# Kernel tuning notes

Hardware: AMD Instinct MI355X
Metric: run time of the kernel (lower is better)

## Reference

```python
import jax, jax.numpy as jnp
import numpy as np

LATENT, HIDDEN, OUT = 256, 1024, 512
B, T = 32, 512
NUM_LAYERS = 3


def setup_inputs() -> dict:
    key = jax.random.key(0)
    ks = jax.random.split(key, 16)
    init = lambda k, shape, fan: (jax.random.normal(k, shape, jnp.float32) / np.sqrt(fan)).astype(jnp.float32)
    seq_lens = jnp.sort(jax.random.randint(ks[2], (B,), 1, T + 1)).at[-1].set(T)
    inp = {
        "z": jax.random.normal(ks[0], (B, LATENT), jnp.float32),
        "seq_lens": seq_lens,
        "chord_embedding": jax.random.normal(ks[1], (B, T, HIDDEN), jnp.float32),
        "fc_w": init(ks[3], (HIDDEN, LATENT), LATENT),
        "fc_b": jnp.zeros((HIDDEN,), jnp.float32),
    }
    in_dims = [HIDDEN, OUT, OUT]
    for l in range(NUM_LAYERS):
        inp[f"w_ih{l}"] = init(ks[4 + 2 * l], (3 * OUT, in_dims[l]), in_dims[l])
        inp[f"w_hh{l}"] = init(ks[5 + 2 * l], (3 * OUT, OUT), OUT)
        inp[f"b_ih{l}"] = jnp.zeros((3 * OUT,), jnp.float32)
        inp[f"b_hh{l}"] = jnp.zeros((3 * OUT,), jnp.float32)
    return inp


def _gru_layer(x, w_ih, w_hh, b_ih, b_hh):
    # x: [B, T, in_dim] -> [B, T, H]; PyTorch gate order: r, z, n
    Bb, Tt, _ = x.shape
    H = w_hh.shape[1]
    gx = jnp.einsum('bti,gi->btg', x, w_ih) + b_ih  # [B, T, 3H] batched GEMM

    def step(h, gx_t):
        gh = h @ w_hh.T + b_hh                      # [B, 3H]
        xr, xz, xn = jnp.split(gx_t, 3, axis=-1)
        hr, hz, hn = jnp.split(gh, 3, axis=-1)
        r = jax.nn.sigmoid(xr + hr)
        zg = jax.nn.sigmoid(xz + hz)
        n = jnp.tanh(xn + r * hn)
        h_new = (1.0 - zg) * n + zg * h
        return h_new, h_new

    h0 = jnp.zeros((Bb, H), x.dtype)
    _, ys = jax.lax.scan(step, h0, jnp.swapaxes(gx, 0, 1))  # scan over time
    return jnp.swapaxes(ys, 0, 1)


def reference(z, seq_lens, chord_embedding, fc_w, fc_b,
              w_ih0, w_hh0, b_ih0, b_hh0,
              w_ih1, w_hh1, b_ih1, b_hh1,
              w_ih2, w_hh2, b_ih2, b_hh2):
    # FC + ReLU, broadcast over time, add scaled chord embedding
    h = jax.nn.relu(z @ fc_w.T + fc_b)[:, None, :]          # [B, 1, HIDDEN]
    x = h + chord_embedding / 100.0                          # [B, T, HIDDEN]
    # 3-layer GRU, batched over all samples at once. GRU is causal, so running
    # the full padded sequence and masking t >= seq_len equals the original
    # per-sample truncated loop (positions < seq_len are bitwise identical).
    x = _gru_layer(x, w_ih0, w_hh0, b_ih0, b_hh0)
    x = _gru_layer(x, w_ih1, w_hh1, b_ih1, b_hh1)
    x = _gru_layer(x, w_ih2, w_hh2, b_ih2, b_hh2)
    mask = (jnp.arange(x.shape[1])[None, :] < seq_lens[:, None]).astype(x.dtype)
    return x * mask[:, :, None]                              # [B, T, OUT], zero-padded
```

## Files before the change

### kernel.cpp

```cpp
#include <hip/hip_runtime.h>
#include <hip/hip_bf16.h>
#include <stdint.h>

#define LATENT 256
#define HIDDEN 1024
#define GOUT 512
#define NB 32
#define TT 512
#define G3 1536

typedef float f32x4 __attribute__((ext_vector_type(4)));
typedef short s16x8 __attribute__((ext_vector_type(8)));
typedef uint32_t u32;
typedef unsigned long long u64;

#define GLP(p) ((const __attribute__((address_space(1))) u32*)(p))
#define LLP(p) ((__attribute__((address_space(3))) u32*)(p))

__device__ __forceinline__ short f2bf(float f) {
  u32 u = __builtin_bit_cast(u32, f);
  u32 r = (u + 0x7FFFu + ((u >> 16) & 1u)) >> 16;
  return (short)r;
}
__device__ __forceinline__ float bf2f(short s) {
  u32 u = ((u32)(unsigned short)s) << 16;
  return __builtin_bit_cast(float, u);
}
__device__ __forceinline__ u32 pk2(float a, float b) {
  return (u32)(unsigned short)f2bf(a) | ((u32)(unsigned short)f2bf(b) << 16);
}
__device__ __forceinline__ s16x8 f2bf8(float4 a, float4 b) {
  s16x8 r;
  r[0] = f2bf(a.x); r[1] = f2bf(a.y); r[2] = f2bf(a.z); r[3] = f2bf(a.w);
  r[4] = f2bf(b.x); r[5] = f2bf(b.y); r[6] = f2bf(b.z); r[7] = f2bf(b.w);
  return r;
}
__device__ __forceinline__ float ldgx(const float* p) { return *p; }
__device__ __forceinline__ float ldgx(const short* p) { return bf2f(*p); }

__global__ __launch_bounds__(256) void fc_kernel(const float* __restrict__ z,
                                                 const float* __restrict__ fc_w,
                                                 const float* __restrict__ fc_b,
                                                 float* __restrict__ hfc) {
  __shared__ float zs[LATENT];
  int tid = threadIdx.x;
  int gid = blockIdx.x * 256 + tid;
  int b = gid >> 10, j = gid & 1023;
  zs[tid] = z[b * LATENT + tid];
  __syncthreads();
  const float4* wr = (const float4*)(fc_w + (size_t)j * LATENT);
  float s = 0.f;
#pragma unroll
  for (int k = 0; k < LATENT / 4; ++k) {
    float4 wv = wr[k];
    float4 zv = *(const float4*)&zs[k * 4];
    s += wv.x * zv.x + wv.y * zv.y + wv.z * zv.z + wv.w * zv.w;
  }
  s += fc_b[j];
  hfc[gid] = fmaxf(s, 0.f);
}

__global__ __launch_bounds__(256) void x0_kernel(const float* __restrict__ hfc,
                                                 const float* __restrict__ chord,
                                                 short* __restrict__ x0) {
  int r = blockIdx.x;
  int b = r & 31, t = r >> 5;
  int k = threadIdx.x * 4;
  float4 c = *(const float4*)(chord + ((size_t)b * TT + t) * HIDDEN + k);
  float4 h = *(const float4*)(hfc + (size_t)b * HIDDEN + k);
  u32 p0 = pk2(h.x + c.x * 0.01f, h.y + c.y * 0.01f);
  u32 p1 = pk2(h.z + c.z * 0.01f, h.w + c.w * 0.01f);
  uint2 pv; pv.x = p0; pv.y = p1;
  *(uint2*)(x0 + (size_t)r * HIDDEN + k) = pv;
}

__global__ __launch_bounds__(256) void cvt_kernel(const float* __restrict__ src,
                                                  short* __restrict__ dst, int n4) {
  int i = blockIdx.x * 256 + threadIdx.x;
  if (i < n4) {
    float4 v = ((const float4*)src)[i];
    uint2 pv; pv.x = pk2(v.x, v.y); pv.y = pk2(v.z, v.w);
    ((uint2*)dst)[i] = pv;
  }
}

template <typename OutT>
__global__ __launch_bounds__(256) void gemm_bt(const short* __restrict__ A,
                                               const short* __restrict__ Bw,
                                               OutT* __restrict__ C, int M, int N, int K) {
  __shared__ short As[128 * 32];
  __shared__ short Bs[128 * 32];
  const int tid = threadIdx.x;
  const int lane = tid & 63, wave = tid >> 6;
  const int l15 = lane & 15, quad = lane >> 4;
  const int n0 = blockIdx.x * 128, m0 = blockIdx.y * 128;
  const int wm = (wave >> 1) * 64, wn = (wave & 1) * 64;
  f32x4 acc[4][4] = {};
  for (int k0 = 0; k0 < K; k0 += 32) {
#pragma unroll
    for (int c = 0; c < 2; ++c) {
      int idx = c * 256 + tid;
      int row = idx >> 2, cs = (idx & 3) * 8;
      const u32* ga = (const u32*)(A + (size_t)(m0 + row) * K + k0 + cs);
      const u32* gb = (const u32*)(Bw + (size_t)(n0 + row) * K + k0 + cs);
      u32* sa = (u32*)As + (size_t)(c * 256 + wave * 64) * 4;
      u32* sb = (u32*)Bs + (size_t)(c * 256 + wave * 64) * 4;
      __builtin_amdgcn_global_load_lds(GLP(ga), LLP(sa), 16, 0, 0);
      __builtin_amdgcn_global_load_lds(GLP(gb), LLP(sb), 16, 0, 0);
    }
    __syncthreads();
    s16x8 af[4], bfr[4];
#pragma unroll
    for (int i = 0; i < 4; ++i)
      af[i] = *(const s16x8*)(As + (wm + i * 16 + l15) * 32 + quad * 8);
#pragma unroll
    for (int j = 0; j < 4; ++j)
      bfr[j] = *(const s16x8*)(Bs + (wn + j * 16 + l15) * 32 + quad * 8);
#pragma unroll
    for (int i = 0; i < 4; ++i)
#pragma unroll
      for (int j = 0; j < 4; ++j)
        acc[i][j] = __builtin_amdgcn_mfma_f32_16x16x32_bf16(af[i], bfr[j], acc[i][j], 0, 0, 0);
    __syncthreads();
  }
#pragma unroll
  for (int i = 0; i < 4; ++i)
#pragma unroll
    for (int j = 0; j < 4; ++j)
#pragma unroll
      for (int r = 0; r < 4; ++r) {
        int m = m0 + wm + i * 16 + quad * 4 + r;
        int n = n0 + wn + j * 16 + l15;
        float v = acc[i][j][r];
        if constexpr (__is_same(OutT, float)) C[(size_t)m * N + n] = v;
        else C[(size_t)m * N + n] = f2bf(v);
      }
}

template <typename GxT>
__global__ __launch_bounds__(512) void gru_layer(const GxT* __restrict__ gx,
                                                 const float* __restrict__ w_hh,
                                                 const float* __restrict__ b_ih,
                                                 const float* __restrict__ b_hh,
                                                 u64* __restrict__ h_buf,
                                                 int tag_base,
                                                 short* __restrict__ x_out,
                                                 float* __restrict__ f_out,
                                                 const int* __restrict__ seq_lens) {
  const int bid = blockIdx.x;
  const int g = bid & 7, wg = bid >> 3;
  const int u0 = wg * 32;
  const int tid = threadIdx.x, lane = tid & 63, wave = tid >> 6;
  const int l15 = lane & 15, quad = lane >> 4;
  __shared__ u32 h_lds[4 * 256];
  __shared__ float lds_c[3 * 4 * 32];

  u64* hb = h_buf + (size_t)g * 2048;

  const int gate = wave >> 1, half = wave & 1;
  s16x8 wfrag[16];
  if (wave < 6) {
    const int col = gate * 512 + u0 + half * 16 + l15;
#pragma unroll
    for (int kb = 0; kb < 16; ++kb) {
      const float* p = w_hh + (size_t)col * 512 + kb * 32 + quad * 8;
      wfrag[kb] = f2bf8(*(const float4*)p, *(const float4*)(p + 4));
    }
  }

  const bool is_c = (wave >= 6);
  const int ci = tid - 384;
  const int cb = ci >> 5, cu = ci & 31;
  const int gbat = g * 4 + cb, u = u0 + cu;
  float bihr = 0, bihz = 0, bihn = 0, bhhr = 0, bhhz = 0, bhhn = 0;
  int slen = 0;
  float hprev = 0.f, pgx[3] = {0.f, 0.f, 0.f};
  if (is_c) {
    bihr = b_ih[u]; bihz = b_ih[512 + u]; bihn = b_ih[1024 + u];
    bhhr = b_hh[u]; bhhz = b_hh[512 + u]; bhhn = b_hh[1024 + u];
    slen = seq_lens[gbat];
#pragma unroll
    for (int gs = 0; gs < 3; ++gs)
      pgx[gs] = ldgx(&gx[(size_t)gbat * G3 + gs * 512 + u]);
  }

  const int w0 = tid * 2;
  const int srow = w0 >> 8, sc = w0 & 255;
  const int saddr = srow * 256 + (sc ^ (srow * 4) ^ ((srow & 1) * 16));

  for (int t = 0; t < TT; ++t) {
    if (t > 0) {
      const u32 want = (u32)(tag_base + t);
      u64* src = hb + ((t - 1) & 1) * 1024;
      u64 v0 = __hip_atomic_load(src + w0, __ATOMIC_RELAXED, __HIP_MEMORY_SCOPE_AGENT);
      u64 v1 = __hip_atomic_load(src + w0 + 1, __ATOMIC_RELAXED, __HIP_MEMORY_SCOPE_AGENT);
      while ((u32)(v0 >> 32) != want)
        v0 = __hip_atomic_load(src + w0, __ATOMIC_RELAXED, __HIP_MEMORY_SCOPE_AGENT);
      while ((u32)(v1 >> 32) != want)
        v1 = __hip_atomic_load(src + w0 + 1, __ATOMIC_RELAXED, __HIP_MEMORY_SCOPE_AGENT);
      uint2 pw; pw.x = (u32)v0; pw.y = (u32)v1;
      *(uint2*)&h_lds[saddr] = pw;
    }
    __syncthreads();

    if (wave < 6) {
      f32x4 a0 = {0.f, 0.f, 0.f, 0.f}, a1 = a0, a2 = a0, a3 = a0;
      if (t > 0) {
        const int r = l15 & 3;
        const int rsw = r * 4, rhi = (r & 1) * 16;
#pragma unroll
        for (int kb = 0; kb < 16; ++kb) {
          s16x8 a = *(const s16x8*)&h_lds[r * 256 + ((kb * 16 + quad * 4) ^ rsw ^ rhi)];
          if ((kb & 3) == 0)      a0 = __builtin_amdgcn_mfma_f32_16x16x32_bf16(a, wfrag[kb], a0, 0, 0, 0);
          else if ((kb & 3) == 1) a1 = __builtin_amdgcn_mfma_f32_16x16x32_bf16(a, wfrag[kb], a1, 0, 0, 0);
          else if ((kb & 3) == 2) a2 = __builtin_amdgcn_mfma_f32_16x16x32_bf16(a, wfrag[kb], a2, 0, 0, 0);
          else                    a3 = __builtin_amdgcn_mfma_f32_16x16x32_bf16(a, wfrag[kb], a3, 0, 0, 0);
        }
      }
      if (quad == 0) {
        const int uc = half * 16 + l15;
#pragma unroll
        for (int r = 0; r < 4; ++r)
          lds_c[gate * 128 + r * 32 + uc] = (a0[r] + a1[r]) + (a2[r] + a3[r]);
      }
    }
    __syncthreads();

    if (is_c) {
      float ghr = lds_c[0 * 128 + cb * 32 + cu];
      float ghz = lds_c[1 * 128 + cb * 32 + cu];
      float ghn = lds_c[2 * 128 + cb * 32 + cu];
      float cr = pgx[0], cz = pgx[1], cn = pgx[2];
      if (t + 1 < TT) {
#pragma unroll
        for (int gs = 0; gs < 3; ++gs)
          pgx[gs] = ldgx(&gx[(size_t)((t + 1) * NB + gbat) * G3 + gs * 512 + u]);
      }
      float xr = cr + bihr + ghr + bhhr;
      float xz = cz + bihz + ghz + bhhz;
      float rr = 1.f / (1.f + __expf(-xr));
      float zz = 1.f / (1.f + __expf(-xz));
      float pre = cn + bihn + rr * (ghn + bhhn);
      float ax = fabsf(pre);
      float e = __expf(-2.f * ax);
      float nn = copysignf((1.f - e) / (1.f + e), pre);
      float h = (1.f - zz) * nn + zz * hprev;
      hprev = h;
      float other = __shfl_xor(h, 1);
      if (!(tid & 1)) {
        u64 val = (u64)pk2(h, other) | (((u64)(u32)(tag_base + t + 1)) << 32);
        __hip_atomic_store(hb + (t & 1) * 1024 + cb * 256 + (u >> 1), val,
                           __ATOMIC_RELAXED, __HIP_MEMORY_SCOPE_AGENT);
      }
      if (x_out) x_out[(size_t)(t * NB + gbat) * 512 + u] = f2bf(h);
      if (f_out) f_out[((size_t)gbat * TT + t) * 512 + u] = (t < slen) ? h : 0.f;
    }
  }
}

extern "C" void kernel_launch(void* const* d_in, const int* in_sizes, int n_in,
                              void* d_out, int out_size, void* d_ws, size_t ws_size,
                              hipStream_t stream) {
  (void)in_sizes; (void)n_in; (void)out_size;
  const float* z       = (const float*)d_in[0];
  const int*   seq     = (const int*)d_in[1];
  const float* chord   = (const float*)d_in[2];
  const float* fc_w    = (const float*)d_in[3];
  const float* fc_b    = (const float*)d_in[4];
  const float* w_ih[3] = {(const float*)d_in[5], (const float*)d_in[9],  (const float*)d_in[13]};
  const float* w_hh[3] = {(const float*)d_in[6], (const float*)d_in[10], (const float*)d_in[14]};
  const float* b_ih[3] = {(const float*)d_in[7], (const float*)d_in[11], (const float*)d_in[15]};
  const float* b_hh[3] = {(const float*)d_in[8], (const float*)d_in[12], (const float*)d_in[16]};

  char* w = (char*)d_ws;
  size_t off = 0;
  auto alloc = [&](size_t bytes) -> void* {
    void* p = w + off;
    off = (off + bytes + 255) & ~(size_t)255;
    return p;
  };
  u64*   hbuf = (u64*)alloc((size_t)8 * 2048 * 8);
  float* hfc  = (float*)alloc((size_t)NB * HIDDEN * 4);
  short* x0   = (short*)alloc((size_t)TT * NB * HIDDEN * 2);
  short* x1   = (short*)alloc((size_t)TT * NB * GOUT * 2);
  short* w0b  = (short*)alloc((size_t)G3 * HIDDEN * 2);
  short* w1b  = (short*)alloc((size_t)G3 * GOUT * 2);
  short* w2b  = (short*)alloc((size_t)G3 * GOUT * 2);
  size_t fixed = off;
  bool gx_f32 = (fixed + (size_t)TT * NB * G3 * 4) <= ws_size;
  void* gx = alloc(gx_f32 ? (size_t)TT * NB * G3 * 4 : (size_t)TT * NB * G3 * 2);

  fc_kernel<<<128, 256, 0, stream>>>(z, fc_w, fc_b, hfc);
  x0_kernel<<<TT * NB, 256, 0, stream>>>(hfc, chord, x0);
  cvt_kernel<<<(G3 * HIDDEN / 4 + 255) / 256, 256, 0, stream>>>(w_ih[0], w0b, G3 * HIDDEN / 4);
  cvt_kernel<<<(G3 * GOUT / 4 + 255) / 256, 256, 0, stream>>>(w_ih[1], w1b, G3 * GOUT / 4);
  cvt_kernel<<<(G3 * GOUT / 4 + 255) / 256, 256, 0, stream>>>(w_ih[2], w2b, G3 * GOUT / 4);

  dim3 gg(G3 / 128, TT * NB / 128);
  if (gx_f32) {
    float* gxf = (float*)gx;
    gemm_bt<float><<<gg, 256, 0, stream>>>(x0, w0b, gxf, TT * NB, G3, HIDDEN);
    gru_layer<float><<<128, 512, 0, stream>>>(gxf, w_hh[0], b_ih[0], b_hh[0], hbuf, 0 * 1024, x1, nullptr, seq);
    gemm_bt<float><<<gg, 256, 0, stream>>>(x1, w1b, gxf, TT * NB, G3, GOUT);
    gru_layer<float><<<128, 512, 0, stream>>>(gxf, w_hh[1], b_ih[1], b_hh[1], hbuf, 1 * 1024, x1, nullptr, seq);
    gemm_bt<float><<<gg, 256, 0, stream>>>(x1, w2b, gxf, TT * NB, G3, GOUT);
    gru_layer<float><<<128, 512, 0, stream>>>(gxf, w_hh[2], b_ih[2], b_hh[2], hbuf, 2 * 1024, nullptr, (float*)d_out, seq);
  } else {
    short* gxb = (short*)gx;
    gemm_bt<short><<<gg, 256, 0, stream>>>(x0, w0b, gxb, TT * NB, G3, HIDDEN);
    gru_layer<short><<<128, 512, 0, stream>>>(gxb, w_hh[0], b_ih[0], b_hh[0], hbuf, 0 * 1024, x1, nullptr, seq);
    gemm_bt<short><<<gg, 256, 0, stream>>>(x1, w1b, gxb, TT * NB, G3, GOUT);
    gru_layer<short><<<128, 512, 0, stream>>>(gxb, w_hh[1], b_ih[1], b_hh[1], hbuf, 1 * 1024, x1, nullptr, seq);
    gemm_bt<short><<<gg, 256, 0, stream>>>(x1, w2b, gxb, TT * NB, G3, GOUT);
    gru_layer<short><<<128, 512, 0, stream>>>(gxb, w_hh[2], b_ih[2], b_hh[2], hbuf, 2 * 1024, nullptr, (float*)d_out, seq);
  }
}
```

Measured before the change: 2.700 ms.

## Fuse three GRU layers into one wavefront-pipelined persistent kernel

Replaces the three sequential GRU layer kernels and the two intermediate input-projection GEMMs with one persistent kernel of 96 blocks, 32 per layer. Each layer consumes the previous layer's hidden state per timestep through tagged ring buffers with 4 slots, and layers 1-2 compute their input projection on the fly with MFMA in spare waves. This lets the layers run as a time-skewed pipeline instead of serially and drops the gx round trips to global memory. Blocks now cover 16 batch rows, so each step has fewer cross-block exchanges. In exchange it relies on all 96 blocks being co-resident, adds backpressure spinning, and increases LDS and register pressure.

```diff
diff --git a/kernel.cpp b/kernel.cpp
--- a/kernel.cpp
+++ b/kernel.cpp
@@ -37,6 +37,9 @@
 }
 __device__ __forceinline__ float ldgx(const float* p) { return *p; }
 __device__ __forceinline__ float ldgx(const short* p) { return bf2f(*p); }
+__device__ __forceinline__ u64 ald(const u64* p) {
+  return __hip_atomic_load(p, __ATOMIC_RELAXED, __HIP_MEMORY_SCOPE_AGENT);
+}
 
 __global__ __launch_bounds__(256) void fc_kernel(const float* __restrict__ z,
                                                  const float* __restrict__ fc_w,
@@ -137,123 +140,210 @@
       }
 }
 
+
+struct GruP {
+  const float* w_hh[3];
+  const float* w_ih[3];
+  const float* b_ih[3];
+  const float* b_hh[3];
+};
+
+#define SLOT_WORDS 4096
+#define HB_WORDS  (4 * SLOT_WORDS)
+
+__global__ __launch_bounds__(256) void clr_kernel(u64* __restrict__ p) {
+  p[(size_t)blockIdx.x * 256 + threadIdx.x] = 0ull;
+}
+
 template <typename GxT>
-__global__ __launch_bounds__(512) void gru_layer(const GxT* __restrict__ gx,
-                                                 const float* __restrict__ w_hh,
-                                                 const float* __restrict__ b_ih,
-                                                 const float* __restrict__ b_hh,
-                                                 u64* __restrict__ h_buf,
-                                                 int tag_base,
-                                                 short* __restrict__ x_out,
-                                                 float* __restrict__ f_out,
-                                                 const int* __restrict__ seq_lens) {
+__global__ __launch_bounds__(1024) void gru3(GruP P,
+                                             const GxT* __restrict__ gx0,
+                                             u64* __restrict__ hbc,
+                                             const int* __restrict__ seq,
+                                             float* __restrict__ out) {
   const int bid = blockIdx.x;
-  const int g = bid & 7, wg = bid >> 3;
+  const int layer = bid >> 5;
+  const int g = bid & 1;
+  const int wg = (bid >> 1) & 15;
   const int u0 = wg * 32;
-  const int tid = threadIdx.x, lane = tid & 63, wave = tid >> 6;
+  const int tid = threadIdx.x;
+  const int lane = tid & 63, wave = tid >> 6;
   const int l15 = lane & 15, quad = lane >> 4;
-  __shared__ u32 h_lds[4 * 256];
-  __shared__ float lds_c[3 * 4 * 32];
-
-  u64* hb = h_buf + (size_t)g * 2048;
-
-  const int gate = wave >> 1, half = wave & 1;
+
+  __shared__ u32 h_lds[16 * 256];
+  __shared__ u32 x_lds[16 * 256];
+  __shared__ float gh_c[3 * 512];
+  __shared__ float gx_c[3 * 512];
+
+  u64* hb_own = hbc + (size_t)(layer * 2 + g) * HB_WORDS;
+  const u64* hb_prev = (layer > 0) ? hbc + (size_t)((layer - 1) * 2 + g) * HB_WORDS : hbc;
+  const u64* hb_next = (layer < 2) ? hbc + (size_t)((layer + 1) * 2 + g) * HB_WORDS : hbc;
+
+  const bool is_hh = (wave < 6);
+  const bool do_ih = (wave >= 6 && wave < 12 && layer > 0);
+  const bool is_c  = (wave >= 12);
+
+  int gate = 0, half = 0;
   s16x8 wfrag[16];
-  if (wave < 6) {
+  if (is_hh || do_ih) {
+    const int wv = is_hh ? wave : wave - 6;
+    gate = wv >> 1; half = wv & 1;
+    const float* W = is_hh ? P.w_hh[layer] : P.w_ih[layer];
     const int col = gate * 512 + u0 + half * 16 + l15;
 #pragma unroll
     for (int kb = 0; kb < 16; ++kb) {
-      const float* p = w_hh + (size_t)col * 512 + kb * 32 + quad * 8;
+      const float* p = W + (size_t)col * 512 + kb * 32 + quad * 8;
       wfrag[kb] = f2bf8(*(const float4*)p, *(const float4*)(p + 4));
     }
   }
 
-  const bool is_c = (wave >= 6);
-  const int ci = tid - 384;
-  const int cb = ci >> 5, cu = ci & 31;
-  const int gbat = g * 4 + cb, u = u0 + cu;
-  float bihr = 0, bihz = 0, bihn = 0, bhhr = 0, bhhz = 0, bhhn = 0;
-  int slen = 0;
-  float hprev = 0.f, pgx[3] = {0.f, 0.f, 0.f};
+  const int ci0 = tid - 768;
+  float bih[2][3], bhh[2][3], pgx[2][3], hprev[2];
+  int slen[2];
+  hprev[0] = hprev[1] = 0.f; slen[0] = slen[1] = 0;
+#pragma unroll
+  for (int p = 0; p < 2; ++p)
+#pragma unroll
+    for (int gs = 0; gs < 3; ++gs) { bih[p][gs] = 0.f; bhh[p][gs] = 0.f; pgx[p][gs] = 0.f; }
   if (is_c) {
-    bihr = b_ih[u]; bihz = b_ih[512 + u]; bihn = b_ih[1024 + u];
-    bhhr = b_hh[u]; bhhz = b_hh[512 + u]; bhhn = b_hh[1024 + u];
-    slen = seq_lens[gbat];
-#pragma unroll
-    for (int gs = 0; gs < 3; ++gs)
-      pgx[gs] = ldgx(&gx[(size_t)gbat * G3 + gs * 512 + u]);
-  }
-
-  const int w0 = tid * 2;
-  const int srow = w0 >> 8, sc = w0 & 255;
-  const int saddr = srow * 256 + (sc ^ (srow * 4) ^ ((srow & 1) * 16));
+#pragma unroll
+    for (int p = 0; p < 2; ++p) {
+      const int ci = ci0 + p * 256;
+      const int cu = ci & 31, cb = ci >> 5;
+      const int u = u0 + cu, gb = g * 16 + cb;
+#pragma unroll
+      for (int gs = 0; gs < 3; ++gs) {
+        bih[p][gs] = P.b_ih[layer][gs * 512 + u];
+        bhh[p][gs] = P.b_hh[layer][gs * 512 + u];
+      }
+      slen[p] = seq[gb];
+      if (layer == 0) {
+#pragma unroll
+        for (int gs = 0; gs < 3; ++gs)
+          pgx[p][gs] = ldgx(&gx0[(size_t)gb * G3 + gs * 512 + u]);
+      }
+    }
+  }
+
+  const int w0 = tid * 4;
+  const int srow = w0 >> 8;
+  const int saddr = srow * 256 + ((w0 & 255) ^ (srow << 2));
 
   for (int t = 0; t < TT; ++t) {
+    const bool chk = (layer < 2 && t >= 4 && tid < 16);
+    const u64* cw = hb_next + (size_t)(t & 3) * SLOT_WORDS + tid * 16;
+    u64 cv = 0;
+    if (chk) cv = ald(cw);
+    const u64* hsrc = hb_own + (size_t)((t - 1) & 3) * SLOT_WORDS + w0;
+    u64 hv0 = 0, hv1 = 0, hv2 = 0, hv3 = 0;
+    if (t > 0) { hv0 = ald(hsrc); hv1 = ald(hsrc + 1); hv2 = ald(hsrc + 2); hv3 = ald(hsrc + 3); }
+    const u64* xsrc = hb_prev + (size_t)(t & 3) * SLOT_WORDS + w0;
+    u64 xv0 = 0, xv1 = 0, xv2 = 0, xv3 = 0;
+    if (layer > 0) { xv0 = ald(xsrc); xv1 = ald(xsrc + 1); xv2 = ald(xsrc + 2); xv3 = ald(xsrc + 3); }
+
+    if (chk) {
+      const u32 wt = (u32)(t - 3);
+      while ((int)((u32)(cv >> 32) - wt) < 0) cv = ald(cw);
+    }
     if (t > 0) {
-      const u32 want = (u32)(tag_base + t);
-      u64* src = hb + ((t - 1) & 1) * 1024;
-      u64 v0 = __hip_atomic_load(src + w0, __ATOMIC_RELAXED, __HIP_MEMORY_SCOPE_AGENT);
-      u64 v1 = __hip_atomic_load(src + w0 + 1, __ATOMIC_RELAXED, __HIP_MEMORY_SCOPE_AGENT);
-      while ((u32)(v0 >> 32) != want)
-        v0 = __hip_atomic_load(src + w0, __ATOMIC_RELAXED, __HIP_MEMORY_SCOPE_AGENT);
-      while ((u32)(v1 >> 32) != want)
-        v1 = __hip_atomic_load(src + w0 + 1, __ATOMIC_RELAXED, __HIP_MEMORY_SCOPE_AGENT);
-      uint2 pw; pw.x = (u32)v0; pw.y = (u32)v1;
-      *(uint2*)&h_lds[saddr] = pw;
+      const u32 wt = (u32)t;
+      while ((u32)(hv0 >> 32) != wt) hv0 = ald(hsrc);
+      while ((u32)(hv1 >> 32) != wt) hv1 = ald(hsrc + 1);
+      while ((u32)(hv2 >> 32) != wt) hv2 = ald(hsrc + 2);
+      while ((u32)(hv3 >> 32) != wt) hv3 = ald(hsrc + 3);
+      uint4 pw; pw.x = (u32)hv0; pw.y = (u32)hv1; pw.z = (u32)hv2; pw.w = (u32)hv3;
+      *(uint4*)&h_lds[saddr] = pw;
+    }
+    if (layer > 0) {
+      const u32 wt = (u32)(t + 1);
+      while ((u32)(xv0 >> 32) != wt) xv0 = ald(xsrc);
+      while ((u32)(xv1 >> 32) != wt) xv1 = ald(xsrc + 1);
+      while ((u32)(xv2 >> 32) != wt) xv2 = ald(xsrc + 2);
+      while ((u32)(xv3 >> 32) != wt) xv3 = ald(xsrc + 3);
+      uint4 pw; pw.x = (u32)xv0; pw.y = (u32)xv1; pw.z = (u32)xv2; pw.w = (u32)xv3;
+      *(uint4*)&x_lds[saddr] = pw;
     }
     __syncthreads();
 
-    if (wave < 6) {
+    if (is_hh) {
       f32x4 a0 = {0.f, 0.f, 0.f, 0.f}, a1 = a0, a2 = a0, a3 = a0;
       if (t > 0) {
-        const int r = l15 & 3;
-        const int rsw = r * 4, rhi = (r & 1) * 16;
+        const int rb = l15 * 256, rx = l15 << 2;
 #pragma unroll
         for (int kb = 0; kb < 16; ++kb) {
-          s16x8 a = *(const s16x8*)&h_lds[r * 256 + ((kb * 16 + quad * 4) ^ rsw ^ rhi)];
+          s16x8 a = *(const s16x8*)&h_lds[rb + ((kb * 16 + quad * 4) ^ rx)];
           if ((kb & 3) == 0)      a0 = __builtin_amdgcn_mfma_f32_16x16x32_bf16(a, wfrag[kb], a0, 0, 0, 0);
           else if ((kb & 3) == 1) a1 = __builtin_amdgcn_mfma_f32_16x16x32_bf16(a, wfrag[kb], a1, 0, 0, 0);
           else if ((kb & 3) == 2) a2 = __builtin_amdgcn_mfma_f32_16x16x32_bf16(a, wfrag[kb], a2, 0, 0, 0);
           else                    a3 = __builtin_amdgcn_mfma_f32_16x16x32_bf16(a, wfrag[kb], a3, 0, 0, 0);
         }
       }
-      if (quad == 0) {
-        const int uc = half * 16 + l15;
-#pragma unroll
-        for (int r = 0; r < 4; ++r)
-          lds_c[gate * 128 + r * 32 + uc] = (a0[r] + a1[r]) + (a2[r] + a3[r]);
-      }
+      const int uc = half * 16 + l15;
+#pragma unroll
+      for (int r = 0; r < 4; ++r)
+        gh_c[gate * 512 + (quad * 4 + r) * 32 + uc] = (a0[r] + a1[r]) + (a2[r] + a3[r]);
+    } else if (do_ih) {
+      f32x4 a0 = {0.f, 0.f, 0.f, 0.f}, a1 = a0, a2 = a0, a3 = a0;
+      const int rb = l15 * 256, rx = l15 << 2;
+#pragma unroll
+      for (int kb = 0; kb < 16; ++kb) {
+        s16x8 a = *(const s16x8*)&x_lds[rb + ((kb * 16 + quad * 4) ^ rx)];
+        if ((kb & 3) == 0)      a0 = __builtin_amdgcn_mfma_f32_16x16x32_bf16(a, wfrag[kb], a0, 0, 0, 0);
+        else if ((kb & 3) == 1) a1 = __builtin_amdgcn_mfma_f32_16x16x32_bf16(a, wfrag[kb], a1, 0, 0, 0);
+        else if ((kb & 3) == 2) a2 = __builtin_amdgcn_mfma_f32_16x16x32_bf16(a, wfrag[kb], a2, 0, 0, 0);
+        else                    a3 = __builtin_amdgcn_mfma_f32_16x16x32_bf16(a, wfrag[kb], a3, 0, 0, 0);
+      }
+      const int uc = half * 16 + l15;
+#pragma unroll
+      for (int r = 0; r < 4; ++r)
+        gx_c[gate * 512 + (quad * 4 + r) * 32 + uc] = (a0[r] + a1[r]) + (a2[r] + a3[r]);
     }
     __syncthreads();
 
     if (is_c) {
-      float ghr = lds_c[0 * 128 + cb * 32 + cu];
-      float ghz = lds_c[1 * 128 + cb * 32 + cu];
-      float ghn = lds_c[2 * 128 + cb * 32 + cu];
-      float cr = pgx[0], cz = pgx[1], cn = pgx[2];
-      if (t + 1 < TT) {
-#pragma unroll
-        for (int gs = 0; gs < 3; ++gs)
-          pgx[gs] = ldgx(&gx[(size_t)((t + 1) * NB + gbat) * G3 + gs * 512 + u]);
-      }
-      float xr = cr + bihr + ghr + bhhr;
-      float xz = cz + bihz + ghz + bhhz;
-      float rr = 1.f / (1.f + __expf(-xr));
-      float zz = 1.f / (1.f + __expf(-xz));
-      float pre = cn + bihn + rr * (ghn + bhhn);
-      float ax = fabsf(pre);
-      float e = __expf(-2.f * ax);
-      float nn = copysignf((1.f - e) / (1.f + e), pre);
-      float h = (1.f - zz) * nn + zz * hprev;
-      hprev = h;
-      float other = __shfl_xor(h, 1);
-      if (!(tid & 1)) {
-        u64 val = (u64)pk2(h, other) | (((u64)(u32)(tag_base + t + 1)) << 32);
-        __hip_atomic_store(hb + (t & 1) * 1024 + cb * 256 + (u >> 1), val,
-                           __ATOMIC_RELAXED, __HIP_MEMORY_SCOPE_AGENT);
-      }
-      if (x_out) x_out[(size_t)(t * NB + gbat) * 512 + u] = f2bf(h);
-      if (f_out) f_out[((size_t)gbat * TT + t) * 512 + u] = (t < slen) ? h : 0.f;
+      float hs[2];
+#pragma unroll
+      for (int p = 0; p < 2; ++p) {
+        const int ci = ci0 + p * 256;
+        const int cu = ci & 31, cb = ci >> 5;
+        const int u = u0 + cu, gb = g * 16 + cb;
+        float cr, cz, cn;
+        if (layer == 0) {
+          cr = pgx[p][0]; cz = pgx[p][1]; cn = pgx[p][2];
+          if (t + 1 < TT) {
+#pragma unroll
+            for (int gs = 0; gs < 3; ++gs)
+              pgx[p][gs] = ldgx(&gx0[(size_t)((t + 1) * NB + gb) * G3 + gs * 512 + u]);
+          }
+        } else {
+          cr = gx_c[ci]; cz = gx_c[512 + ci]; cn = gx_c[1024 + ci];
+        }
+        const float ghr = gh_c[ci], ghz = gh_c[512 + ci], ghn = gh_c[1024 + ci];
+        const float xr = cr + bih[p][0] + ghr + bhh[p][0];
+        const float xz = cz + bih[p][1] + ghz + bhh[p][1];
+        const float rr = 1.f / (1.f + __expf(-xr));
+        const float zz = 1.f / (1.f + __expf(-xz));
+        const float pre = cn + bih[p][2] + rr * (ghn + bhh[p][2]);
+        const float ax = fabsf(pre);
+        const float e = __expf(-2.f * ax);
+        const float nn = copysignf((1.f - e) / (1.f + e), pre);
+        const float h = (1.f - zz) * nn + zz * hprev[p];
+        hprev[p] = h; hs[p] = h;
+        if (layer == 2) out[((size_t)gb * TT + t) * 512 + u] = (t < slen[p]) ? h : 0.f;
+      }
+      u64* dst = hb_own + (size_t)(t & 3) * SLOT_WORDS;
+      const u64 tg = ((u64)(u32)(t + 1)) << 32;
+#pragma unroll
+      for (int p = 0; p < 2; ++p) {
+        const float other = __shfl_xor(hs[p], 1);
+        if (!(lane & 1)) {
+          const int ci = ci0 + p * 256;
+          const int cb = ci >> 5;
+          const int u = u0 + (ci & 31);
+          __hip_atomic_store(dst + cb * 256 + (u >> 1), (u64)pk2(hs[p], other) | tg,
+                             __ATOMIC_RELAXED, __HIP_MEMORY_SCOPE_AGENT);
+        }
+      }
     }
   }
 }
@@ -262,15 +352,17 @@
                               void* d_out, int out_size, void* d_ws, size_t ws_size,
                               hipStream_t stream) {
   (void)in_sizes; (void)n_in; (void)out_size;
-  const float* z       = (const float*)d_in[0];
-  const int*   seq     = (const int*)d_in[1];
-  const float* chord   = (const float*)d_in[2];
-  const float* fc_w    = (const float*)d_in[3];
-  const float* fc_b    = (const float*)d_in[4];
-  const float* w_ih[3] = {(const float*)d_in[5], (const float*)d_in[9],  (const float*)d_in[13]};
-  const float* w_hh[3] = {(const float*)d_in[6], (const float*)d_in[10], (const float*)d_in[14]};
-  const float* b_ih[3] = {(const float*)d_in[7], (const float*)d_in[11], (const float*)d_in[15]};
-  const float* b_hh[3] = {(const float*)d_in[8], (const float*)d_in[12], (const float*)d_in[16]};
+  const float* z     = (const float*)d_in[0];
+  const int*   seq   = (const int*)d_in[1];
+  const float* chord = (const float*)d_in[2];
+  const float* fc_w  = (const float*)d_in[3];
+  const float* fc_b  = (const float*)d_in[4];
+  GruP P;
+  const float* w_ih0 = (const float*)d_in[5];
+  P.w_ih[0] = w_ih0;
+  P.w_hh[0] = (const float*)d_in[6];  P.b_ih[0] = (const float*)d_in[7];  P.b_hh[0] = (const float*)d_in[8];
+  P.w_ih[1] = (const float*)d_in[9];  P.w_hh[1] = (const float*)d_in[10]; P.b_ih[1] = (const float*)d_in[11]; P.b_hh[1] = (const float*)d_in[12];
+  P.w_ih[2] = (const float*)d_in[13]; P.w_hh[2] = (const float*)d_in[14]; P.b_ih[2] = (const float*)d_in[15]; P.b_hh[2] = (const float*)d_in[16];
 
   char* w = (char*)d_ws;
   size_t off = 0;
@@ -279,39 +371,27 @@
     off = (off + bytes + 255) & ~(size_t)255;
     return p;
   };
-  u64*   hbuf = (u64*)alloc((size_t)8 * 2048 * 8);
-  float* hfc  = (float*)alloc((size_t)NB * HIDDEN * 4);
-  short* x0   = (short*)alloc((size_t)TT * NB * HIDDEN * 2);
-  short* x1   = (short*)alloc((size_t)TT * NB * GOUT * 2);
-  short* w0b  = (short*)alloc((size_t)G3 * HIDDEN * 2);
-  short* w1b  = (short*)alloc((size_t)G3 * GOUT * 2);
-  short* w2b  = (short*)alloc((size_t)G3 * GOUT * 2);
+  u64*   hbc = (u64*)alloc((size_t)6 * HB_WORDS * 8);
+  float* hfc = (float*)alloc((size_t)NB * HIDDEN * 4);
+  short* x0  = (short*)alloc((size_t)TT * NB * HIDDEN * 2);
+  short* w0b = (short*)alloc((size_t)G3 * HIDDEN * 2);
   size_t fixed = off;
   bool gx_f32 = (fixed + (size_t)TT * NB * G3 * 4) <= ws_size;
   void* gx = alloc(gx_f32 ? (size_t)TT * NB * G3 * 4 : (size_t)TT * NB * G3 * 2);
 
+  clr_kernel<<<(6 * HB_WORDS) / 256, 256, 0, stream>>>(hbc);
   fc_kernel<<<128, 256, 0, stream>>>(z, fc_w, fc_b, hfc);
   x0_kernel<<<TT * NB, 256, 0, stream>>>(hfc, chord, x0);
-  cvt_kernel<<<(G3 * HIDDEN / 4 + 255) / 256, 256, 0, stream>>>(w_ih[0], w0b, G3 * HIDDEN / 4);
-  cvt_kernel<<<(G3 * GOUT / 4 + 255) / 256, 256, 0, stream>>>(w_ih[1], w1b, G3 * GOUT / 4);
-  cvt_kernel<<<(G3 * GOUT / 4 + 255) / 256, 256, 0, stream>>>(w_ih[2], w2b, G3 * GOUT / 4);
+  cvt_kernel<<<(G3 * HIDDEN / 4 + 255) / 256, 256, 0, stream>>>(w_ih0, w0b, G3 * HIDDEN / 4);
 
   dim3 gg(G3 / 128, TT * NB / 128);
   if (gx_f32) {
     float* gxf = (float*)gx;
     gemm_bt<float><<<gg, 256, 0, stream>>>(x0, w0b, gxf, TT * NB, G3, HIDDEN);
-    gru_layer<float><<<128, 512, 0, stream>>>(gxf, w_hh[0], b_ih[0], b_hh[0], hbuf, 0 * 1024, x1, nullptr, seq);
-    gemm_bt<float><<<gg, 256, 0, stream>>>(x1, w1b, gxf, TT * NB, G3, GOUT);
-    gru_layer<float><<<128, 512, 0, stream>>>(gxf, w_hh[1], b_ih[1], b_hh[1], hbuf, 1 * 1024, x1, nullptr, seq);
-    gemm_bt<float><<<gg, 256, 0, stream>>>(x1, w2b, gxf, TT * NB, G3, GOUT);
-    gru_layer<float><<<128, 512, 0, stream>>>(gxf, w_hh[2], b_ih[2], b_hh[2], hbuf, 2 * 1024, nullptr, (float*)d_out, seq);
+    gru3<float><<<96, 1024, 0, stream>>>(P, gxf, hbc, seq, (float*)d_out);
   } else {
     short* gxb = (short*)gx;
     gemm_bt<short><<<gg, 256, 0, stream>>>(x0, w0b, gxb, TT * NB, G3, HIDDEN);
-    gru_layer<short><<<128, 512, 0, stream>>>(gxb, w_hh[0], b_ih[0], b_hh[0], hbuf, 0 * 1024, x1, nullptr, seq);
-    gemm_bt<short><<<gg, 256, 0, stream>>>(x1, w1b, gxb, TT * NB, G3, GOUT);
-    gru_layer<short><<<128, 512, 0, stream>>>(gxb, w_hh[1], b_ih[1], b_hh[1], hbuf, 1 * 1024, x1, nullptr, seq);
-    gemm_bt<short><<<gg, 256, 0, stream>>>(x1, w2b, gxb, TT * NB, G3, GOUT);
-    gru_layer<short><<<128, 512, 0, stream>>>(gxb, w_hh[2], b_ih[2], b_hh[2], hbuf, 2 * 1024, nullptr, (float*)d_out, seq);
-  }
-}
+    gru3<short><<<96, 1024, 0, stream>>>(P, gxb, hbc, seq, (float*)d_out);
+  }
+}
```

Measured after the change: 3.621 ms. +34.1%, slower.

## Restructure GRU recurrence into single-wave blocks polling global h directly into MFMA

Applied to the files above, without the earlier changes.

Replaces the 512-thread GRU block, which staged h in LDS and used two block barriers per step, with 64-thread single-wave blocks. Each wave owns 16 hidden units for all three gates and 16 batches, and keeps its 48 W_hh fragments in registers. Tagged h words are polled from global memory straight into MFMA operands in a staggered order, with no LDS and no __syncthreads. Blocks are spread across XCDs (only indices 0 and 4 are active) and a clear kernel zeroes the h buffer. The aim is to cut per-step barrier and LDS latency on the serial critical path, at the cost of heavy register pressure and more global spin-loads per step.

```diff
diff --git a/kernel.cpp b/kernel.cpp
--- a/kernel.cpp
+++ b/kernel.cpp
@@ -37,6 +37,9 @@
 }
 __device__ __forceinline__ float ldgx(const float* p) { return *p; }
 __device__ __forceinline__ float ldgx(const short* p) { return bf2f(*p); }
+__device__ __forceinline__ u64 ald(const u64* p) {
+  return __hip_atomic_load(p, __ATOMIC_RELAXED, __HIP_MEMORY_SCOPE_AGENT);
+}
 
 __global__ __launch_bounds__(256) void fc_kernel(const float* __restrict__ z,
                                                  const float* __restrict__ fc_w,
@@ -137,123 +140,130 @@
       }
 }
 
+__global__ __launch_bounds__(256) void clr_kernel(u64* __restrict__ p) {
+  p[(size_t)blockIdx.x * 256 + threadIdx.x] = 0ull;
+}
+
 template <typename GxT>
-__global__ __launch_bounds__(512) void gru_layer(const GxT* __restrict__ gx,
-                                                 const float* __restrict__ w_hh,
-                                                 const float* __restrict__ b_ih,
-                                                 const float* __restrict__ b_hh,
-                                                 u64* __restrict__ h_buf,
-                                                 int tag_base,
-                                                 short* __restrict__ x_out,
-                                                 float* __restrict__ f_out,
-                                                 const int* __restrict__ seq_lens) {
+__global__ __launch_bounds__(64) void gru_seq(const GxT* __restrict__ gx,
+                                              const float* __restrict__ w_hh,
+                                              const float* __restrict__ b_ih,
+                                              const float* __restrict__ b_hh,
+                                              u64* __restrict__ h_buf,
+                                              int tb,
+                                              short* __restrict__ x_out,
+                                              float* __restrict__ f_out,
+                                              const int* __restrict__ seq_lens) {
   const int bid = blockIdx.x;
-  const int g = bid & 7, wg = bid >> 3;
-  const int u0 = wg * 32;
-  const int tid = threadIdx.x, lane = tid & 63, wave = tid >> 6;
+  const int xs = bid & 7;
+  int g;
+  if (xs == 0) g = 0;
+  else if (xs == 4) g = 1;
+  else return;
+  const int wq = bid >> 3;
+  const int u0 = wq * 16;
+  const int lane = threadIdx.x;
   const int l15 = lane & 15, quad = lane >> 4;
-  __shared__ u32 h_lds[4 * 256];
-  __shared__ float lds_c[3 * 4 * 32];
-
-  u64* hb = h_buf + (size_t)g * 2048;
-
-  const int gate = wave >> 1, half = wave & 1;
-  s16x8 wfrag[16];
-  if (wave < 6) {
-    const int col = gate * 512 + u0 + half * 16 + l15;
-#pragma unroll
-    for (int kb = 0; kb < 16; ++kb) {
-      const float* p = w_hh + (size_t)col * 512 + kb * 32 + quad * 8;
-      wfrag[kb] = f2bf8(*(const float4*)p, *(const float4*)(p + 4));
-    }
-  }
-
-  const bool is_c = (wave >= 6);
-  const int ci = tid - 384;
-  const int cb = ci >> 5, cu = ci & 31;
-  const int gbat = g * 4 + cb, u = u0 + cu;
-  float bihr = 0, bihz = 0, bihn = 0, bhhr = 0, bhhz = 0, bhhn = 0;
-  int slen = 0;
-  float hprev = 0.f, pgx[3] = {0.f, 0.f, 0.f};
-  if (is_c) {
-    bihr = b_ih[u]; bihz = b_ih[512 + u]; bihn = b_ih[1024 + u];
-    bhhr = b_hh[u]; bhhz = b_hh[512 + u]; bhhn = b_hh[1024 + u];
-    slen = seq_lens[gbat];
-#pragma unroll
-    for (int gs = 0; gs < 3; ++gs)
-      pgx[gs] = ldgx(&gx[(size_t)gbat * G3 + gs * 512 + u]);
-  }
-
-  const int w0 = tid * 2;
-  const int srow = w0 >> 8, sc = w0 & 255;
-  const int saddr = srow * 256 + (sc ^ (srow * 4) ^ ((srow & 1) * 16));
+  const int u = u0 + l15;
+
+  u64* hb = h_buf + (size_t)g * 8192;
+  const int st = wq & 15;
+
+  s16x8 wf[48];
+#pragma unroll
+  for (int i = 0; i < 16; ++i) {
+    const int kb = (st + i) & 15;
+#pragma unroll
+    for (int gt = 0; gt < 3; ++gt) {
+      const float* p = w_hh + (size_t)(gt * 512 + u) * 512 + kb * 32 + quad * 8;
+      wf[gt * 16 + i] = f2bf8(*(const float4*)p, *(const float4*)(p + 4));
+    }
+  }
+
+  const float bihr = b_ih[u], bihz = b_ih[512 + u], bihn = b_ih[1024 + u];
+  const float bhhr = b_hh[u], bhhz = b_hh[512 + u], bhhn = b_hh[1024 + u];
+
+  float hprev[4] = {0.f, 0.f, 0.f, 0.f};
+  int slen[4] = {0, 0, 0, 0};
+  float pgx[3][4];
+#pragma unroll
+  for (int r = 0; r < 4; ++r) {
+    const int gb = g * 16 + quad * 4 + r;
+    if (f_out) slen[r] = seq_lens[gb];
+#pragma unroll
+    for (int gt = 0; gt < 3; ++gt)
+      pgx[gt][r] = ldgx(&gx[(size_t)gb * G3 + gt * 512 + u]);
+  }
 
   for (int t = 0; t < TT; ++t) {
+    f32x4 ar = {0.f, 0.f, 0.f, 0.f}, az = ar, an = ar;
     if (t > 0) {
-      const u32 want = (u32)(tag_base + t);
-      u64* src = hb + ((t - 1) & 1) * 1024;
-      u64 v0 = __hip_atomic_load(src + w0, __ATOMIC_RELAXED, __HIP_MEMORY_SCOPE_AGENT);
-      u64 v1 = __hip_atomic_load(src + w0 + 1, __ATOMIC_RELAXED, __HIP_MEMORY_SCOPE_AGENT);
-      while ((u32)(v0 >> 32) != want)
-        v0 = __hip_atomic_load(src + w0, __ATOMIC_RELAXED, __HIP_MEMORY_SCOPE_AGENT);
-      while ((u32)(v1 >> 32) != want)
-        v1 = __hip_atomic_load(src + w0 + 1, __ATOMIC_RELAXED, __HIP_MEMORY_SCOPE_AGENT);
-      uint2 pw; pw.x = (u32)v0; pw.y = (u32)v1;
-      *(uint2*)&h_lds[saddr] = pw;
-    }
-    __syncthreads();
-
-    if (wave < 6) {
-      f32x4 a0 = {0.f, 0.f, 0.f, 0.f}, a1 = a0, a2 = a0, a3 = a0;
-      if (t > 0) {
-        const int r = l15 & 3;
-        const int rsw = r * 4, rhi = (r & 1) * 16;
-#pragma unroll
-        for (int kb = 0; kb < 16; ++kb) {
-          s16x8 a = *(const s16x8*)&h_lds[r * 256 + ((kb * 16 + quad * 4) ^ rsw ^ rhi)];
-          if ((kb & 3) == 0)      a0 = __builtin_amdgcn_mfma_f32_16x16x32_bf16(a, wfrag[kb], a0, 0, 0, 0);
-          else if ((kb & 3) == 1) a1 = __builtin_amdgcn_mfma_f32_16x16x32_bf16(a, wfrag[kb], a1, 0, 0, 0);
-          else if ((kb & 3) == 2) a2 = __builtin_amdgcn_mfma_f32_16x16x32_bf16(a, wfrag[kb], a2, 0, 0, 0);
-          else                    a3 = __builtin_amdgcn_mfma_f32_16x16x32_bf16(a, wfrag[kb], a3, 0, 0, 0);
+      const u64* sb = hb + ((t - 1) & 1) * 4096 + l15 * 256 + quad * 4;
+      const u32 want = (u32)(tb + t);
+      u64 pw[4][4];
+#pragma unroll
+      for (int p = 0; p < 4; ++p) {
+        const u64* a = sb + ((st + p) & 15) * 16;
+        pw[p][0] = ald(a); pw[p][1] = ald(a + 1); pw[p][2] = ald(a + 2); pw[p][3] = ald(a + 3);
+      }
+#pragma unroll
+      for (int i = 0; i < 16; ++i) {
+        const int p = i & 3;
+        const u64* a = sb + ((st + i) & 15) * 16;
+        u64 v0 = pw[p][0], v1 = pw[p][1], v2 = pw[p][2], v3 = pw[p][3];
+        while (((((u32)(v0 >> 32)) ^ want) | (((u32)(v1 >> 32)) ^ want) |
+                (((u32)(v2 >> 32)) ^ want) | (((u32)(v3 >> 32)) ^ want)) != 0u) {
+          v0 = ald(a); v1 = ald(a + 1); v2 = ald(a + 2); v3 = ald(a + 3);
+        }
+        uint4 uu; uu.x = (u32)v0; uu.y = (u32)v1; uu.z = (u32)v2; uu.w = (u32)v3;
+        const s16x8 fr = __builtin_bit_cast(s16x8, uu);
+        ar = __builtin_amdgcn_mfma_f32_16x16x32_bf16(fr, wf[i],      ar, 0, 0, 0);
+        az = __builtin_amdgcn_mfma_f32_16x16x32_bf16(fr, wf[16 + i], az, 0, 0, 0);
+        an = __builtin_amdgcn_mfma_f32_16x16x32_bf16(fr, wf[32 + i], an, 0, 0, 0);
+        if (i < 12) {
+          const u64* a2 = sb + ((st + i + 4) & 15) * 16;
+          pw[p][0] = ald(a2); pw[p][1] = ald(a2 + 1); pw[p][2] = ald(a2 + 2); pw[p][3] = ald(a2 + 3);
         }
       }
-      if (quad == 0) {
-        const int uc = half * 16 + l15;
-#pragma unroll
-        for (int r = 0; r < 4; ++r)
-          lds_c[gate * 128 + r * 32 + uc] = (a0[r] + a1[r]) + (a2[r] + a3[r]);
-      }
-    }
-    __syncthreads();
-
-    if (is_c) {
-      float ghr = lds_c[0 * 128 + cb * 32 + cu];
-      float ghz = lds_c[1 * 128 + cb * 32 + cu];
-      float ghn = lds_c[2 * 128 + cb * 32 + cu];
-      float cr = pgx[0], cz = pgx[1], cn = pgx[2];
-      if (t + 1 < TT) {
-#pragma unroll
-        for (int gs = 0; gs < 3; ++gs)
-          pgx[gs] = ldgx(&gx[(size_t)((t + 1) * NB + gbat) * G3 + gs * 512 + u]);
-      }
-      float xr = cr + bihr + ghr + bhhr;
-      float xz = cz + bihz + ghz + bhhz;
-      float rr = 1.f / (1.f + __expf(-xr));
-      float zz = 1.f / (1.f + __expf(-xz));
-      float pre = cn + bihn + rr * (ghn + bhhn);
-      float ax = fabsf(pre);
-      float e = __expf(-2.f * ax);
-      float nn = copysignf((1.f - e) / (1.f + e), pre);
-      float h = (1.f - zz) * nn + zz * hprev;
-      hprev = h;
-      float other = __shfl_xor(h, 1);
-      if (!(tid & 1)) {
-        u64 val = (u64)pk2(h, other) | (((u64)(u32)(tag_base + t + 1)) << 32);
-        __hip_atomic_store(hb + (t & 1) * 1024 + cb * 256 + (u >> 1), val,
+    }
+
+    float hs[4];
+#pragma unroll
+    for (int r = 0; r < 4; ++r) {
+      const float xr = pgx[0][r] + bihr + ar[r] + bhhr;
+      const float xz = pgx[1][r] + bihz + az[r] + bhhz;
+      const float rr = 1.f / (1.f + __expf(-xr));
+      const float zz = 1.f / (1.f + __expf(-xz));
+      const float pre = pgx[2][r] + bihn + rr * (an[r] + bhhn);
+      const float ax = fabsf(pre);
+      const float e = __expf(-2.f * ax);
+      const float nn = copysignf((1.f - e) / (1.f + e), pre);
+      const float h = (1.f - zz) * nn + zz * hprev[r];
+      hprev[r] = h; hs[r] = h;
+    }
+    u64* dst = hb + (t & 1) * 4096;
+    const u64 tg = ((u64)(u32)(tb + t + 1)) << 32;
+#pragma unroll
+    for (int r = 0; r < 4; ++r) {
+      const float other = __shfl_xor(hs[r], 1);
+      if (!(lane & 1))
+        __hip_atomic_store(dst + (quad * 4 + r) * 256 + (u >> 1), (u64)pk2(hs[r], other) | tg,
                            __ATOMIC_RELAXED, __HIP_MEMORY_SCOPE_AGENT);
-      }
-      if (x_out) x_out[(size_t)(t * NB + gbat) * 512 + u] = f2bf(h);
-      if (f_out) f_out[((size_t)gbat * TT + t) * 512 + u] = (t < slen) ? h : 0.f;
+    }
+    if (t + 1 < TT) {
+#pragma unroll
+      for (int gt = 0; gt < 3; ++gt)
+#pragma unroll
+        for (int r = 0; r < 4; ++r) {
+          const int gb = g * 16 + quad * 4 + r;
+          pgx[gt][r] = ldgx(&gx[(size_t)((t + 1) * NB + gb) * G3 + gt * 512 + u]);
+        }
+    }
+#pragma unroll
+    for (int r = 0; r < 4; ++r) {
+      const int gb = g * 16 + quad * 4 + r;
+      if (x_out) x_out[(size_t)(t * NB + gb) * 512 + u] = f2bf(hs[r]);
+      if (f_out) f_out[((size_t)gb * TT + t) * 512 + u] = (t < slen[r]) ? hs[r] : 0.f;
     }
   }
 }
@@ -279,7 +289,7 @@
     off = (off + bytes + 255) & ~(size_t)255;
     return p;
   };
-  u64*   hbuf = (u64*)alloc((size_t)8 * 2048 * 8);
+  u64*   hbuf = (u64*)alloc((size_t)2 * 8192 * 8);
   float* hfc  = (float*)alloc((size_t)NB * HIDDEN * 4);
   short* x0   = (short*)alloc((size_t)TT * NB * HIDDEN * 2);
   short* x1   = (short*)alloc((size_t)TT * NB * GOUT * 2);
@@ -290,6 +300,7 @@
   bool gx_f32 = (fixed + (size_t)TT * NB * G3 * 4) <= ws_size;
   void* gx = alloc(gx_f32 ? (size_t)TT * NB * G3 * 4 : (size_t)TT * NB * G3 * 2);
 
+  clr_kernel<<<64, 256, 0, stream>>>(hbuf);
   fc_kernel<<<128, 256, 0, stream>>>(z, fc_w, fc_b, hfc);
   x0_kernel<<<TT * NB, 256, 0, stream>>>(hfc, chord, x0);
   cvt_kernel<<<(G3 * HIDDEN / 4 + 255) / 256, 256, 0, stream>>>(w_ih[0], w0b, G3 * HIDDEN / 4);
@@ -300,18 +311,18 @@
   if (gx_f32) {
     float* gxf = (float*)gx;
     gemm_bt<float><<<gg, 256, 0, stream>>>(x0, w0b, gxf, TT * NB, G3, HIDDEN);
-    gru_layer<float><<<128, 512, 0, stream>>>(gxf, w_hh[0], b_ih[0], b_hh[0], hbuf, 0 * 1024, x1, nullptr, seq);
+    gru_seq<float><<<256, 64, 0, stream>>>(gxf, w_hh[0], b_ih[0], b_hh[0], hbuf, 0 * 1024, x1, nullptr, seq);
     gemm_bt<float><<<gg, 256, 0, stream>>>(x1, w1b, gxf, TT * NB, G3, GOUT);
-    gru_layer<float><<<128, 512, 0, stream>>>(gxf, w_hh[1], b_ih[1], b_hh[1], hbuf, 1 * 1024, x1, nullptr, seq);
+    gru_seq<float><<<256, 64, 0, stream>>>(gxf, w_hh[1], b_ih[1], b_hh[1], hbuf, 1 * 1024, x1, nullptr, seq);
     gemm_bt<float><<<gg, 256, 0, stream>>>(x1, w2b, gxf, TT * NB, G3, GOUT);
-    gru_layer<float><<<128, 512, 0, stream>>>(gxf, w_hh[2], b_ih[2], b_hh[2], hbuf, 2 * 1024, nullptr, (float*)d_out, seq);
+    gru_seq<float><<<256, 64, 0, stream>>>(gxf, w_hh[2], b_ih[2], b_hh[2], hbuf, 2 * 1024, nullptr, (float*)d_out, seq);
   } else {
     short* gxb = (short*)gx;
     gemm_bt<short><<<gg, 256, 0, stream>>>(x0, w0b, gxb, TT * NB, G3, HIDDEN);
-    gru_layer<short><<<128, 512, 0, stream>>>(gxb, w_hh[0], b_ih[0], b_hh[0], hbuf, 0 * 1024, x1, nullptr, seq);
+    gru_seq<short><<<256, 64, 0, stream>>>(gxb, w_hh[0], b_ih[0], b_hh[0], hbuf, 0 * 1024, x1, nullptr, seq);
     gemm_bt<short><<<gg, 256, 0, stream>>>(x1, w1b, gxb, TT * NB, G3, GOUT);
-    gru_layer<short><<<128, 512, 0, stream>>>(gxb, w_hh[1], b_ih[1], b_hh[1], hbuf, 1 * 1024, x1, nullptr, seq);
+    gru_seq<short><<<256, 64, 0, stream>>>(gxb, w_hh[1], b_ih[1], b_hh[1], hbuf, 1 * 1024, x1, nullptr, seq);
     gemm_bt<short><<<gg, 256, 0, stream>>>(x1, w2b, gxb, TT * NB, G3, GOUT);
-    gru_layer<short><<<128, 512, 0, stream>>>(gxb, w_hh[2], b_ih[2], b_hh[2], hbuf, 2 * 1024, nullptr, (float*)d_out, seq);
-  }
-}
+    gru_seq<short><<<256, 64, 0, stream>>>(gxb, w_hh[2], b_ih[2], b_hh[2], hbuf, 2 * 1024, nullptr, (float*)d_out, seq);
+  }
+}
```

New measurement: 5.453 ms. 2.02x slower.
